# Kernel optimization log

Hardware: AMD Instinct MI355X
Metric: run time of the kernel (lower is better)

The kernel has to match this reference:

```python
import jax, jax.numpy as jnp
import numpy as np

TEMPERATURE = 0.1
NUM_RISK_GROUPS = 4
SIM_WEIGHT = 1.0
CONTRAST_WEIGHT = 0.1
NEG = jnp.float32(-1e9)  # finite stand-in for -inf (grad-safe, exp() == 0 in fp32)


def setup_inputs() -> dict:
    key = jax.random.key(0)
    k1, k2, k3, k4 = jax.random.split(key, 4)
    N, D = 8192, 256
    return {
        "log_risks": jax.random.normal(k1, (N,), dtype=jnp.float32),
        "times": jax.random.uniform(k2, (N,), dtype=jnp.float32),
        "censor": jnp.ones((N,), dtype=jnp.int32),
        "wsi_embeddings": jax.random.normal(k3, (N, D), dtype=jnp.float32),
        "omic_embeddings": jax.random.normal(k4, (N, D), dtype=jnp.float32),
    }


def _cox_loss(log_risks, times, censor):
    lr = jnp.clip(log_risks, -10.0, 10.0)
    order = jnp.argsort(-times)  # descending times
    slr = lr[order]
    sc = censor[order]
    # at-risk sum for index i is sum_{j<=i} exp(slr_j) (arange <= i mask) -> cumsum
    at_risk = jnp.cumsum(jnp.exp(slr))
    li = slr - jnp.log(at_risk + 1e-15)
    mask = (sc == 1)
    cnt = jnp.maximum(jnp.sum(mask), 1)
    return -jnp.sum(jnp.where(mask, li, 0.0)) / cnt


def _similarity_loss(a, b):
    na = jnp.maximum(jnp.linalg.norm(a, axis=1), 1e-8)
    nb = jnp.maximum(jnp.linalg.norm(b, axis=1), 1e-8)
    cos = jnp.clip(jnp.sum(a * b, axis=1) / (na * nb), -1.0, 1.0)
    return jnp.mean(1.0 - cos)


def _contrastive_loss(emb, times):
    # NOTE: assumes censor == 1 for all samples (as in setup_inputs), so the
    # uncensored subset is the whole batch and shapes stay static.
    G = NUM_RISK_GROUPS
    q = jnp.quantile(times, jnp.linspace(0.0, 1.0, G + 1))
    # group = #thresholds q[1..G] that t >= ; max bucket clipped to G-1
    groups = jnp.clip(jnp.sum(times[:, None] >= q[None, 1:], axis=1), 0, G - 1)
    z = emb / jnp.maximum(jnp.linalg.norm(emb, axis=1, keepdims=True), 1e-12)
    sim = (z @ z.T) / TEMPERATURE  # [N, N]
    N = emb.shape[0]
    eye = jnp.eye(N, dtype=bool)
    same = groups[:, None] == groups[None, :]
    pos = same & ~eye
    offdiag = ~eye  # pos | neg == all off-diagonal entries
    lse_pos = jax.nn.logsumexp(jnp.where(pos, sim, NEG), axis=1)
    lse_all = jax.nn.logsumexp(jnp.where(offdiag, sim, NEG), axis=1)
    neg_any = jnp.any(~same & ~eye, axis=1)
    valid = jnp.any(pos, axis=1) & neg_any
    loss = -lse_pos + lse_all
    cnt = jnp.maximum(jnp.sum(valid), 1)
    return jnp.sum(jnp.where(valid, loss, 0.0)) / cnt


def reference(log_risks, times, censor, wsi_embeddings, omic_embeddings):
    cox = _cox_loss(log_risks, times, censor)
    sim = _similarity_loss(wsi_embeddings, omic_embeddings)
    c_wsi = _contrastive_loss(wsi_embeddings, times)
    c_omic = _contrastive_loss(omic_embeddings, times)
    contrast = (c_wsi + c_omic) / 2.0
    return cox + SIM_WEIGHT * sim + CONTRAST_WEIGHT * contrast
```

## Files before the change

kernel.cpp:

```cpp
#include <hip/hip_runtime.h>


#define NN 8192
#define DD 256

typedef __attribute__((ext_vector_type(4))) float f32x4;
typedef __attribute__((ext_vector_type(4))) int i32x4;
typedef __attribute__((ext_vector_type(8))) int i32x8;

__device__ inline void gl_lds16(const void* g, void* l) {
  __builtin_amdgcn_global_load_lds(
      (const __attribute__((address_space(1))) unsigned int*)g,
      (__attribute__((address_space(3))) unsigned int*)l, 16, 0, 0);
}

__global__ void __launch_bounds__(256) k_rows(
    const float* __restrict__ lr, const float* __restrict__ times,
    const int* __restrict__ censor,
    const float* __restrict__ wsi, const float* __restrict__ omic,
    unsigned char* __restrict__ pw, unsigned char* __restrict__ po,
    float* __restrict__ pslots, float* __restrict__ gsum) {
  __shared__ __align__(16) float st[1024];
  __shared__ __align__(16) float se[1024];
  __shared__ float red[4][3];
  const int tid = threadIdx.x;
  const int lane = tid & 63;
  const int wv = tid >> 6;
  const int i0 = blockIdx.x * 16 + wv * 4;

  if (blockIdx.x < 64) {
    ((f32x4*)gsum)[blockIdx.x * 256 + tid] = (f32x4){0.f, 0.f, 0.f, 0.f};
  }

  float ti[4];
#pragma unroll
  for (int rr = 0; rr < 4; ++rr) ti[rr] = times[i0 + rr];

  int rk[4] = {0, 0, 0, 0};
  float ar[4] = {0.f, 0.f, 0.f, 0.f};
  for (int c = 0; c < 8; ++c) {
    __syncthreads();
    {
      const float4 t4 = ((const float4*)(times + c * 1024))[tid];
      const float4 l4 = ((const float4*)(lr + c * 1024))[tid];
      ((float4*)st)[tid] = t4;
      float4 e4;
      e4.x = __expf(fminf(fmaxf(l4.x, -10.f), 10.f));
      e4.y = __expf(fminf(fmaxf(l4.y, -10.f), 10.f));
      e4.z = __expf(fminf(fmaxf(l4.z, -10.f), 10.f));
      e4.w = __expf(fminf(fmaxf(l4.w, -10.f), 10.f));
      ((float4*)se)[tid] = e4;
    }
    __syncthreads();
#pragma unroll
    for (int jt = 0; jt < 4; ++jt) {
      const int p = jt * 64 + lane;
      const float4 t = ((const float4*)st)[p];
      const float4 e = ((const float4*)se)[p];
      const int jb = c * 1024 + p * 4;
#define UPD(TV, EV, JJ)                                                  \
  {                                                                      \
    _Pragma("unroll") for (int rr = 0; rr < 4; ++rr) {                   \
      const bool c1 = ((TV) < ti[rr]) ||                                 \
                      (((TV) == ti[rr]) && ((JJ) < i0 + rr));            \
      rk[rr] += c1 ? 1 : 0;                                              \
      ar[rr] += c1 ? 0.f : (EV);                                         \
    }                                                                    \
  }
      UPD(t.x, e.x, jb + 0)
      UPD(t.y, e.y, jb + 1)
      UPD(t.z, e.z, jb + 2)
      UPD(t.w, e.w, jb + 3)
#undef UPD
    }
  }
#pragma unroll
  for (int m = 1; m < 64; m <<= 1) {
#pragma unroll
    for (int rr = 0; rr < 4; ++rr) {
      rk[rr] += __shfl_xor(rk[rr], m);
      ar[rr] += __shfl_xor(ar[rr], m);
    }
  }

  float scox = 0.f, scnt = 0.f, ssim = 0.f;
#pragma unroll
  for (int rr = 0; rr < 4; ++rr) {
    const int i = i0 + rr;
    const float4 w = ((const float4*)(wsi + (size_t)i * DD))[lane];
    const float4 o = ((const float4*)(omic + (size_t)i * DD))[lane];
    float nw = w.x * w.x + w.y * w.y + w.z * w.z + w.w * w.w;
    float no = o.x * o.x + o.y * o.y + o.z * o.z + o.w * o.w;
    float dd = w.x * o.x + w.y * o.y + w.z * o.z + w.w * o.w;
#pragma unroll
    for (int m = 1; m < 64; m <<= 1) {
      nw += __shfl_xor(nw, m);
      no += __shfl_xor(no, m);
      dd += __shfl_xor(dd, m);
    }
    const float nws = sqrtf(nw), nos = sqrtf(no);
    if (lane == 0) {
      float cc = dd / (fmaxf(nws, 1e-8f) * fmaxf(nos, 1e-8f));
      cc = fminf(fmaxf(cc, -1.f), 1.f);
      const float l = fminf(fmaxf(lr[i], -10.f), 10.f);
      const float li = l - logf(ar[rr] + 1e-15f);
      if (censor[i] == 1) { scox += li; scnt += 1.f; }
      ssim += 1.f - cc;
    }
    const float iw = 1.f / fmaxf(nws, 1e-12f);
    const float io = 1.f / fmaxf(nos, 1e-12f);
    int zw = __builtin_amdgcn_cvt_pk_fp8_f32(w.x * iw, w.y * iw, 0, false);
    zw = __builtin_amdgcn_cvt_pk_fp8_f32(w.z * iw, w.w * iw, zw, true);
    int zo = __builtin_amdgcn_cvt_pk_fp8_f32(o.x * io, o.y * io, 0, false);
    zo = __builtin_amdgcn_cvt_pk_fp8_f32(o.z * io, o.w * io, zo, true);
    const size_t off =
        ((size_t)((lane >> 5) * 4 + ((lane >> 3) & 3)) * NN + rk[rr]) * 32 +
        (lane & 7) * 4;
    *(unsigned int*)(pw + off) = (unsigned int)zw;
    *(unsigned int*)(po + off) = (unsigned int)zo;
  }
  if (lane == 0) {
    red[wv][0] = scox; red[wv][1] = scnt; red[wv][2] = ssim;
  }
  __syncthreads();
  if (tid < 3) {
    pslots[blockIdx.x * 4 + tid] =
        red[0][tid] + red[1][tid] + red[2][tid] + red[3][tid];
  }
}

__global__ void __launch_bounds__(256, 4) k_contrast(
    const unsigned char* __restrict__ pw, const unsigned char* __restrict__ po,
    float* __restrict__ gsum) {
  __shared__ __align__(16) unsigned char sbuf[2][16384];
  const int tid = threadIdx.x;
  const int lane = tid & 63;
  const int wv = tid >> 6;
  const int lo = lane & 15, q = lane >> 4;
  const int cb = blockIdx.x, rb = blockIdx.y, mz = blockIdx.z;
  const unsigned char* __restrict__ pk = (mz == 0) ? pw : po;
  const int rowbase = rb * 128 + wv * 32;
  const int colstart = cb * 512;
  const int g = cb >> 2;

  i32x8 afrag[2][2];
#pragma unroll
  for (int rt = 0; rt < 2; ++rt) {
    const size_t row = rowbase + rt * 16 + lo;
#pragma unroll
    for (int ks = 0; ks < 2; ++ks)
      afrag[rt][ks] = *(const i32x8*)(pk + ((size_t)(ks * 4 + q) * NN + row) * 32);
  }

  const unsigned char* gsrc[4];
#pragma unroll
  for (int p = 0; p < 4; ++p) {
    const int u = (wv * 4 + p) * 64 + lane;
    const int uct = u >> 8, uks = (u >> 7) & 1, uh = (u >> 6) & 1;
    const int ul = u & 63;
    gsrc[p] = pk + ((size_t)(uks * 4 + (ul >> 4)) * NN
                    + colstart + uct * 16 + (ul & 15)) * 32 + uh * 16;
  }
  unsigned char* const ldb = &sbuf[0][(size_t)wv * 4096];

#pragma unroll
  for (int p = 0; p < 4; ++p) gl_lds16(gsrc[p], ldb + p * 1024);
  __syncthreads();

  float s[2][4] = {{0.f}};
  const int dctbase = (wv & 1) * 2;

#pragma unroll 1
  for (int st = 0; st < 8; ++st) {
    if (st < 7) {
      const size_t adv = (size_t)(st + 1) * 2048;
      const size_t bofs = ((st + 1) & 1) ? 16384 : 0;
#pragma unroll
      for (int p = 0; p < 4; ++p) gl_lds16(gsrc[p] + adv, ldb + bofs + p * 1024);
    }
    const unsigned char* buf = &sbuf[st & 1][0];
    const bool diagw = ((rowbase >> 6) == ((colstart + st * 64) >> 6));
#pragma unroll
    for (int ct = 0; ct < 4; ++ct) {
      f32x4 a0 = {0.f, 0.f, 0.f, 0.f}, a1 = {0.f, 0.f, 0.f, 0.f};
#pragma unroll
      for (int ks = 0; ks < 2; ++ks) {
        const int rbase = ((ct * 2 + ks) * 2) * 1024 + lane * 16;
        i32x4 blo = *(const i32x4*)&buf[rbase];
        i32x4 bhi = *(const i32x4*)&buf[rbase + 1024];
        i32x8 b = __builtin_shufflevector(blo, bhi, 0, 1, 2, 3, 4, 5, 6, 7);
        a0 = __builtin_amdgcn_mfma_scale_f32_16x16x128_f8f6f4(
            afrag[0][ks], b, a0, 0, 0, 0, 0x7F, 0, 0x7F);
        a1 = __builtin_amdgcn_mfma_scale_f32_16x16x128_f8f6f4(
            afrag[1][ks], b, a1, 0, 0, 0, 0x7F, 0, 0x7F);
      }
      if (diagw) {
#pragma unroll
        for (int r = 0; r < 4; ++r) {
          float e0 = __builtin_amdgcn_exp2f(fmaf(a0[r], 14.4269504f, -14.4269504f));
          float e1 = __builtin_amdgcn_exp2f(fmaf(a1[r], 14.4269504f, -14.4269504f));
          if (ct == dctbase + 0 && lo == q * 4 + r) e0 = 0.f;
          if (ct == dctbase + 1 && lo == q * 4 + r) e1 = 0.f;
          s[0][r] += e0;
          s[1][r] += e1;
        }
      } else {
#pragma unroll
        for (int r = 0; r < 4; ++r) {
          s[0][r] += __builtin_amdgcn_exp2f(fmaf(a0[r], 14.4269504f, -14.4269504f));
          s[1][r] += __builtin_amdgcn_exp2f(fmaf(a1[r], 14.4269504f, -14.4269504f));
        }
      }
    }
    __syncthreads();
  }

#pragma unroll
  for (int rt = 0; rt < 2; ++rt)
#pragma unroll
    for (int r = 0; r < 4; ++r) {
      float v = s[rt][r];
      v += __shfl_xor(v, 1); v += __shfl_xor(v, 2);
      v += __shfl_xor(v, 4); v += __shfl_xor(v, 8);
      if (lo == 0) {
        const int row = rowbase + rt * 16 + q * 4 + r;
        atomicAdd(&gsum[((size_t)mz * NN + row) * 4 + g], v);
      }
    }
}

__global__ void __launch_bounds__(1024) k_finale(
    const float* __restrict__ pslots, const float* __restrict__ gsum,
    float* __restrict__ out) {
  __shared__ float rsum[16][4];
  const int tid = threadIdx.x;
  const int lane = tid & 63, wv = tid >> 6;
  float cox = 0.f, cnt = 0.f, sim = 0.f, con = 0.f;
  for (int b = tid; b < 512; b += 1024) {
    const float4 v = ((const float4*)pslots)[b];
    cox += v.x; cnt += v.y; sim += v.z;
  }
  for (int idx = tid; idx < 2 * NN; idx += 1024) {
    const float4 v = ((const float4*)gsum)[idx];
    const int row = idx & (NN - 1);
    const int gg = row >> 11;
    const float sg = (gg == 0) ? v.x : (gg == 1) ? v.y : (gg == 2) ? v.z : v.w;
    con += logf(v.x + v.y + v.z + v.w) - logf(sg);
  }
  for (int m = 1; m < 64; m <<= 1) {
    cox += __shfl_xor(cox, m);
    cnt += __shfl_xor(cnt, m);
    sim += __shfl_xor(sim, m);
    con += __shfl_xor(con, m);
  }
  if (lane == 0) {
    rsum[wv][0] = cox; rsum[wv][1] = cnt; rsum[wv][2] = sim; rsum[wv][3] = con;
  }
  __syncthreads();
  if (tid == 0) {
    float c0 = 0.f, c1 = 0.f, c2 = 0.f, c3 = 0.f;
    for (int k = 0; k < 16; ++k) {
      c0 += rsum[k][0]; c1 += rsum[k][1]; c2 += rsum[k][2]; c3 += rsum[k][3];
    }
    out[0] = -c0 / fmaxf(c1, 1.f) + c2 / (float)NN
             + 0.1f * 0.5f * c3 / (float)NN;
  }
}

extern "C" void kernel_launch(void* const* d_in, const int* in_sizes, int n_in,
                              void* d_out, int out_size, void* d_ws, size_t ws_size,
                              hipStream_t stream) {
  const float* lr = (const float*)d_in[0];
  const float* times = (const float*)d_in[1];
  const int* censor = (const int*)d_in[2];
  const float* wsi = (const float*)d_in[3];
  const float* omic = (const float*)d_in[4];
  float* out = (float*)d_out;

  char* ws = (char*)d_ws;
  float* pslots = (float*)ws;
  float* gsum = (float*)(ws + 32768);
  unsigned char* pw = (unsigned char*)(ws + 294912);
  unsigned char* po = (unsigned char*)(ws + 294912 + 2097152);

  k_rows<<<512, 256, 0, stream>>>(lr, times, censor, wsi, omic, pw, po, pslots, gsum);
  k_contrast<<<dim3(16, 64, 2), 256, 0, stream>>>(pw, po, gsum);
  k_finale<<<1, 1024, 0, stream>>>(pslots, gsum, out);
}
```

Baseline: 151.5 us.

## Halve rows per wave in rank kernel and drop LDS staging

The rank/at-risk kernel now gives each wave 2 rows instead of 4 and launches 1024 blocks instead of 512, for more parallelism. The LDS tile staging and its two barriers per chunk are removed; each lane reads times and log-risks straight from global memory (likely L2/L1 cached) and recomputes exp itself. The cost is twice the exp work and twice the global reads of the times and log-risks arrays overall. The finale's partial-slot count is updated to match the new block count.

```diff
diff --git a/kernel.cpp b/kernel.cpp
--- a/kernel.cpp
+++ b/kernel.cpp
@@ -20,64 +20,52 @@
     const float* __restrict__ wsi, const float* __restrict__ omic,
     unsigned char* __restrict__ pw, unsigned char* __restrict__ po,
     float* __restrict__ pslots, float* __restrict__ gsum) {
-  __shared__ __align__(16) float st[1024];
-  __shared__ __align__(16) float se[1024];
   __shared__ float red[4][3];
   const int tid = threadIdx.x;
   const int lane = tid & 63;
   const int wv = tid >> 6;
-  const int i0 = blockIdx.x * 16 + wv * 4;
+  const int i0 = blockIdx.x * 8 + wv * 2;
 
   if (blockIdx.x < 64) {
     ((f32x4*)gsum)[blockIdx.x * 256 + tid] = (f32x4){0.f, 0.f, 0.f, 0.f};
   }
 
-  float ti[4];
-#pragma unroll
-  for (int rr = 0; rr < 4; ++rr) ti[rr] = times[i0 + rr];
-
-  int rk[4] = {0, 0, 0, 0};
-  float ar[4] = {0.f, 0.f, 0.f, 0.f};
-  for (int c = 0; c < 8; ++c) {
-    __syncthreads();
-    {
-      const float4 t4 = ((const float4*)(times + c * 1024))[tid];
-      const float4 l4 = ((const float4*)(lr + c * 1024))[tid];
-      ((float4*)st)[tid] = t4;
-      float4 e4;
-      e4.x = __expf(fminf(fmaxf(l4.x, -10.f), 10.f));
-      e4.y = __expf(fminf(fmaxf(l4.y, -10.f), 10.f));
-      e4.z = __expf(fminf(fmaxf(l4.z, -10.f), 10.f));
-      e4.w = __expf(fminf(fmaxf(l4.w, -10.f), 10.f));
-      ((float4*)se)[tid] = e4;
-    }
-    __syncthreads();
-#pragma unroll
-    for (int jt = 0; jt < 4; ++jt) {
-      const int p = jt * 64 + lane;
-      const float4 t = ((const float4*)st)[p];
-      const float4 e = ((const float4*)se)[p];
-      const int jb = c * 1024 + p * 4;
+  float ti[2];
+#pragma unroll
+  for (int rr = 0; rr < 2; ++rr) ti[rr] = times[i0 + rr];
+
+  int rk[2] = {0, 0};
+  float ar[2] = {0.f, 0.f};
+#pragma unroll 4
+  for (int it = 0; it < 32; ++it) {
+    const int p = it * 64 + lane;
+    const float4 t = ((const float4*)times)[p];
+    const float4 l = ((const float4*)lr)[p];
+    float4 e;
+    e.x = __expf(fminf(fmaxf(l.x, -10.f), 10.f));
+    e.y = __expf(fminf(fmaxf(l.y, -10.f), 10.f));
+    e.z = __expf(fminf(fmaxf(l.z, -10.f), 10.f));
+    e.w = __expf(fminf(fmaxf(l.w, -10.f), 10.f));
+    const int jb = p * 4;
 #define UPD(TV, EV, JJ)                                                  \
   {                                                                      \
-    _Pragma("unroll") for (int rr = 0; rr < 4; ++rr) {                   \
+    _Pragma("unroll") for (int rr = 0; rr < 2; ++rr) {                   \
       const bool c1 = ((TV) < ti[rr]) ||                                 \
                       (((TV) == ti[rr]) && ((JJ) < i0 + rr));            \
       rk[rr] += c1 ? 1 : 0;                                              \
       ar[rr] += c1 ? 0.f : (EV);                                         \
     }                                                                    \
   }
-      UPD(t.x, e.x, jb + 0)
-      UPD(t.y, e.y, jb + 1)
-      UPD(t.z, e.z, jb + 2)
-      UPD(t.w, e.w, jb + 3)
+    UPD(t.x, e.x, jb + 0)
+    UPD(t.y, e.y, jb + 1)
+    UPD(t.z, e.z, jb + 2)
+    UPD(t.w, e.w, jb + 3)
 #undef UPD
-    }
   }
 #pragma unroll
   for (int m = 1; m < 64; m <<= 1) {
 #pragma unroll
-    for (int rr = 0; rr < 4; ++rr) {
+    for (int rr = 0; rr < 2; ++rr) {
       rk[rr] += __shfl_xor(rk[rr], m);
       ar[rr] += __shfl_xor(ar[rr], m);
     }
@@ -85,7 +73,7 @@
 
   float scox = 0.f, scnt = 0.f, ssim = 0.f;
 #pragma unroll
-  for (int rr = 0; rr < 4; ++rr) {
+  for (int rr = 0; rr < 2; ++rr) {
     const int i = i0 + rr;
     const float4 w = ((const float4*)(wsi + (size_t)i * DD))[lane];
     const float4 o = ((const float4*)(omic + (size_t)i * DD))[lane];
@@ -236,7 +224,7 @@
   const int tid = threadIdx.x;
   const int lane = tid & 63, wv = tid >> 6;
   float cox = 0.f, cnt = 0.f, sim = 0.f, con = 0.f;
-  for (int b = tid; b < 512; b += 1024) {
+  for (int b = tid; b < 1024; b += 1024) {
     const float4 v = ((const float4*)pslots)[b];
     cox += v.x; cnt += v.y; sim += v.z;
   }
@@ -283,7 +271,7 @@
   unsigned char* pw = (unsigned char*)(ws + 294912);
   unsigned char* po = (unsigned char*)(ws + 294912 + 2097152);
 
-  k_rows<<<512, 256, 0, stream>>>(lr, times, censor, wsi, omic, pw, po, pslots, gsum);
+  k_rows<<<1024, 256, 0, stream>>>(lr, times, censor, wsi, omic, pw, po, pslots, gsum);
   k_contrast<<<dim3(16, 64, 2), 256, 0, stream>>>(pw, po, gsum);
   k_finale<<<1, 1024, 0, stream>>>(pslots, gsum, out);
 }
```

Measured after the change: 145.8 us. -3.8%, faster.
